# Optimization experiments

Hardware: AMD Instinct MI355X
Metric: run time of the kernel (lower is better)

The kernel has to match this reference:

```python
import jax, jax.numpy as jnp
import numpy as np

N_LAYERS = 3
N_HEADS = 8
N_HIDDEN = 16  # hidden_dim // n_heads
HIDDEN = 128
SLOPE = 0.2


def setup_inputs() -> dict:
    key = jax.random.key(0)
    ks = jax.random.split(key, 7)
    B, N, Din, Dh = 4, 512, 2, HIDDEN
    node_features = jax.random.normal(ks[0], (B, N, Din), dtype=jnp.float32)
    adj = jax.random.randint(ks[1], (B, N, N), 0, 2).astype(jnp.int32)
    adj = jnp.maximum(adj, jnp.eye(N, dtype=jnp.int32)[None])  # self loops -> no empty softmax rows
    s = 1.0 / np.sqrt(Dh)
    W_in = jax.random.normal(ks[2], (Din, Dh), dtype=jnp.float32) * (1.0 / np.sqrt(Din))
    W_l = jax.random.normal(ks[3], (N_LAYERS, Dh, N_HEADS * N_HIDDEN), dtype=jnp.float32) * s
    W_r = jax.random.normal(ks[4], (N_LAYERS, Dh, N_HEADS * N_HIDDEN), dtype=jnp.float32) * s
    attn_a = jax.random.normal(ks[5], (N_LAYERS, N_HIDDEN), dtype=jnp.float32) * (1.0 / np.sqrt(N_HIDDEN))
    W_out = jax.random.normal(ks[6], (Dh, 1), dtype=jnp.float32) * s
    return {"node_features": node_features, "adj": adj, "W_in": W_in,
            "W_l": W_l, "W_r": W_r, "attn_a": attn_a, "W_out": W_out}


def _gatv2_layer(h, adj, Wl, Wr, a):
    # h: [B,N,Dh]; adj: [B,N,N] int; Wl/Wr: [Dh, H*F]; a: [F]
    B, N, _ = h.shape
    g_l = (h @ Wl).reshape(B, N, N_HEADS, N_HIDDEN)
    g_r = (h @ Wr).reshape(B, N, N_HEADS, N_HIDDEN)
    # torch: g_sum[b,i,j] = g_l[b,j] + g_r[b,i]  (repeat vs repeat_interleave)
    g_sum = g_r[:, :, None, :, :] + g_l[:, None, :, :, :]  # [B,N,N,H,F]
    e = jnp.einsum('bijhf,f->bijh', jax.nn.leaky_relu(g_sum, SLOPE), a)  # [B,N,N,H]
    e = jnp.where(adj[..., None] == 0, -jnp.inf, e)
    att = jax.nn.softmax(e, axis=2)  # softmax over neighbors j
    out = jnp.einsum('bijh,bjhf->bihf', att, g_r)  # aggregate g_r (per source)
    return out.reshape(B, N, N_HEADS * N_HIDDEN)


def reference(node_features, adj, W_in, W_l, W_r, attn_a, W_out):
    h = node_features @ W_in  # [B,N,128]
    for i in range(N_LAYERS):
        h = _gatv2_layer(h, adj, W_l[i], W_r[i], attn_a[i])
    return h @ W_out  # [B,N,1]
```

## Files before the change

### kernel.cpp

```cpp
#include <hip/hip_runtime.h>
#include <hip/hip_bf16.h>
#include <cstdint>
#include <math.h>

#define NB 4
#define NN 512
#define DH 128
#define NHEADS 8
#define NHID 16
#define SLOPE 0.2f
#define ITILE 32
#define SENTINEL -1e30f

__global__ __launch_bounds__(256) void pack_adj_kernel(
    const int* __restrict__ adj, uint32_t* __restrict__ adjb)
{
    const int t   = threadIdx.x;
    const int row = blockIdx.x * 16 + (t >> 4);
    const int w   = t & 15;
    const int4* p = (const int4*)(adj + (size_t)row * NN + w * 32);
    uint32_t m = 0;
#pragma unroll
    for (int c = 0; c < 8; ++c) {
        const int4 v = p[c];
        m |= (v.x != 0 ? 1u : 0u) << (c * 4 + 0);
        m |= (v.y != 0 ? 1u : 0u) << (c * 4 + 1);
        m |= (v.z != 0 ? 1u : 0u) << (c * 4 + 2);
        m |= (v.w != 0 ? 1u : 0u) << (c * 4 + 3);
    }
    adjb[(size_t)row * 16 + w] = m;
}

__global__ __launch_bounds__(256) void proj_kernel(
    const float* __restrict__ h, const float* __restrict__ X,
    const float* __restrict__ Win,
    const float* __restrict__ Wl, const float* __restrict__ Wr,
    float* __restrict__ gl, float* __restrict__ gr)
{
    __shared__ __align__(16) float s_h[8][DH];
    const int bn0 = blockIdx.x * 8;
    const int b   = bn0 >> 9;
    const int n0  = bn0 & 511;
    const int t   = threadIdx.x;

    if (X) {
        if (t < DH) {
            const float w0 = Win[t], w1 = Win[DH + t];
#pragma unroll
            for (int r = 0; r < 8; ++r) {
                const float x0 = X[(bn0 + r) * 2 + 0];
                const float x1 = X[(bn0 + r) * 2 + 1];
                s_h[r][t] = x0 * w0 + x1 * w1;
            }
        }
    } else {
        for (int idx = t; idx < 8 * DH; idx += 256)
            s_h[idx >> 7][idx & 127] = h[(size_t)bn0 * DH + idx];
    }
    __syncthreads();

    const float* W = (t < DH) ? Wl : Wr;
    float*       g = (t < DH) ? gl : gr;
    const int f128 = t & 127;
    float acc[8] = {};
    for (int k = 0; k < DH; k += 4) {
        const float w0 = W[(k + 0) * DH + f128];
        const float w1 = W[(k + 1) * DH + f128];
        const float w2 = W[(k + 2) * DH + f128];
        const float w3 = W[(k + 3) * DH + f128];
#pragma unroll
        for (int r = 0; r < 8; ++r) {
            const float4 hv = *(const float4*)&s_h[r][k];
            acc[r] += hv.x * w0 + hv.y * w1 + hv.z * w2 + hv.w * w3;
        }
    }
    const int hh = f128 >> 4, f = f128 & 15;
    float* dst = g + ((size_t)(b * NHEADS + hh) * NN + n0) * NHID + f;
#pragma unroll
    for (int r = 0; r < 8; ++r)
        dst[r * NHID] = acc[r];
}

__global__ __launch_bounds__(512) void attn_kernel(
    const float* __restrict__ gl, const float* __restrict__ gr,
    const uint32_t* __restrict__ adjb, const float* __restrict__ a_vec,
    float* __restrict__ h_out,
    const float* __restrict__ Wout, float* __restrict__ out)
{
    __shared__ __align__(16) float smem[17504];
    float* s_gl  = smem;
    float* s_gr  = smem + 8192;
    float* s_acc = smem;
    float* s_m   = smem + 16384;
    float* s_l   = smem + 16912;
    float* s_M   = smem + 17440;
    float* s_inv = smem + 17472;

    const int blk = blockIdx.x;
    const int it  = blk & 15;
    const int bh  = blk >> 4;
    const int b   = bh >> 3;
    const int hh  = bh & 7;
    const int i0  = it * ITILE;
    const int t   = threadIdx.x;
    const int il  = t & 31;
    const int js  = t >> 5;

    {
        const float4* pgl = (const float4*)(gl + (size_t)bh * NN * NHID);
        const float4* pgr = (const float4*)(gr + (size_t)bh * NN * NHID);
        float4* dl = (float4*)s_gl;
        float4* dr = (float4*)s_gr;
#pragma unroll
        for (int k = 0; k < 4; ++k) {
            dl[k * 512 + t] = pgl[k * 512 + t];
            dr[k * 512 + t] = pgr[k * 512 + t];
        }
    }
    float a[16];
    {
        const float4* pa = (const float4*)a_vec;
#pragma unroll
        for (int q = 0; q < 4; ++q) {
            const float4 v = pa[q];
            a[4*q] = v.x; a[4*q+1] = v.y; a[4*q+2] = v.z; a[4*q+3] = v.w;
        }
    }
    const uint32_t mask = adjb[((size_t)(b * NN + i0 + il)) * 16 + js];
    __syncthreads();

    float gri[16];
    {
        const float4* pr = (const float4*)(s_gr + (i0 + il) * NHID);
#pragma unroll
        for (int q = 0; q < 4; ++q) {
            const float4 v = pr[q];
            gri[4*q] = v.x; gri[4*q+1] = v.y; gri[4*q+2] = v.z; gri[4*q+3] = v.w;
        }
    }

    float m = SENTINEL, l = 0.f;
    float acc[16];
#pragma unroll
    for (int f = 0; f < 16; ++f) acc[f] = 0.f;

    const int jbase = js * 32;
    for (int jc = 0; jc < 32; jc += 4) {
        float sc[4];
#pragma unroll
        for (int k = 0; k < 4; ++k) {
            const int jj = jc + k;
            const float4* pg = (const float4*)(s_gl + (jbase + jj) * NHID);
            float s = 0.f;
#pragma unroll
            for (int q = 0; q < 4; ++q) {
                const float4 g = pg[q];
                float v;
                v = g.x + gri[4*q+0]; v = fmaxf(v, SLOPE * v); s += v * a[4*q+0];
                v = g.y + gri[4*q+1]; v = fmaxf(v, SLOPE * v); s += v * a[4*q+1];
                v = g.z + gri[4*q+2]; v = fmaxf(v, SLOPE * v); s += v * a[4*q+2];
                v = g.w + gri[4*q+3]; v = fmaxf(v, SLOPE * v); s += v * a[4*q+3];
            }
            sc[k] = ((mask >> jj) & 1u) ? s : SENTINEL;
        }
        const float m4   = fmaxf(fmaxf(sc[0], sc[1]), fmaxf(sc[2], sc[3]));
        const float newm = fmaxf(m, m4);
        const float corr = __expf(m - newm);
        l *= corr;
#pragma unroll
        for (int f = 0; f < 16; ++f) acc[f] *= corr;
        float p[4];
#pragma unroll
        for (int k = 0; k < 4; ++k) p[k] = __expf(sc[k] - newm);
        l += p[0] + p[1] + p[2] + p[3];
#pragma unroll
        for (int k = 0; k < 4; ++k) {
            const float4* pg = (const float4*)(s_gr + (jbase + jc + k) * NHID);
#pragma unroll
            for (int q = 0; q < 4; ++q) {
                const float4 g = pg[q];
                acc[4*q+0] += p[k] * g.x; acc[4*q+1] += p[k] * g.y;
                acc[4*q+2] += p[k] * g.z; acc[4*q+3] += p[k] * g.w;
            }
        }
        m = newm;
    }

    s_m[js * 33 + il] = m;
    s_l[js * 33 + il] = l;
    __syncthreads();

    if (t < 32) {
        float M = SENTINEL;
#pragma unroll
        for (int k = 0; k < 16; ++k) M = fmaxf(M, s_m[k * 33 + t]);
        float L = 0.f;
#pragma unroll
        for (int k = 0; k < 16; ++k) L += s_l[k * 33 + t] * __expf(s_m[k * 33 + t] - M);
        s_M[t]   = M;
        s_inv[t] = 1.f / L;
    }
    __syncthreads();

    {
        const float scale = __expf(m - s_M[il]) * s_inv[il];
        float* dst = s_acc + (js * 32 + il) * 17;
#pragma unroll
        for (int f = 0; f < 16; ++f) dst[f] = acc[f] * scale;
    }
    __syncthreads();

    {
        const int i = t >> 4, f = t & 15;
        float o = 0.f;
#pragma unroll
        for (int k = 0; k < 16; ++k) o += s_acc[(k * 32 + i) * 17 + f];
        if (Wout) {
            float v = o * Wout[hh * NHID + f];
#pragma unroll
            for (int off = 8; off; off >>= 1) v += __shfl_xor(v, off);
            if (f == 0) atomicAdd(out + b * NN + i0 + i, v);
        } else {
            h_out[((size_t)(b * NN + i0 + i)) * DH + hh * NHID + f] = o;
        }
    }
}

extern "C" void kernel_launch(void* const* d_in, const int* in_sizes, int n_in,
                              void* d_out, int out_size, void* d_ws, size_t ws_size,
                              hipStream_t stream) {
    const float* X    = (const float*)d_in[0];
    const int*   adj  = (const int*)  d_in[1];
    const float* Win  = (const float*)d_in[2];
    const float* Wl   = (const float*)d_in[3];
    const float* Wr   = (const float*)d_in[4];
    const float* Aa   = (const float*)d_in[5];
    const float* Wout = (const float*)d_in[6];
    float* out = (float*)d_out;

    float*    ws   = (float*)d_ws;
    float*    h    = ws;
    float*    gl   = ws + 262144;
    float*    gr   = ws + 524288;
    uint32_t* adjb = (uint32_t*)(ws + 786432);

    pack_adj_kernel<<<NB * NN / 16, 256, 0, stream>>>(adj, adjb);
    hipMemsetAsync(out, 0, (size_t)out_size * sizeof(float), stream);

    for (int l = 0; l < 3; ++l) {
        proj_kernel<<<NB * NN / 8, 256, 0, stream>>>(
            h, (l == 0) ? X : nullptr, Win,
            Wl + (size_t)l * DH * DH, Wr + (size_t)l * DH * DH, gl, gr);
        const bool last = (l == 2);
        attn_kernel<<<NB * NHEADS * (NN / ITILE), 512, 0, stream>>>(
            gl, gr, adjb, Aa + l * NHID, h,
            last ? Wout : nullptr, out);
    }
}
```

Measured before the change: 180.5 us.

## Rewrite GATv2 attention with abs-based leaky-relu, 64-row tiles, two-pass softmax

Uses the identity leaky_relu(v) = 0.6 v + 0.4 |v| (slope 0.2) to pull the linear term out as precomputed per-node dot products with a, leaving only fabs+fma per element. Each thread now handles two query rows (ITILE 64), so each shared-memory g_l/g_r load is reused twice and there are half as many blocks, each reloading the head's g tensors. The online-softmax rescaling is replaced by a plain two-pass max/exp over 32 register-held scores. The final reduction staging uses an XOR-swizzled layout. Register pressure rises (two score arrays of 32 plus two accumulators), and launch_bounds(512,2) may cause spills.

```diff
diff --git a/kernel.cpp b/kernel.cpp
--- a/kernel.cpp
+++ b/kernel.cpp
@@ -1,5 +1,4 @@
 #include <hip/hip_runtime.h>
-#include <hip/hip_bf16.h>
 #include <cstdint>
 #include <math.h>
 
@@ -9,7 +8,7 @@
 #define NHEADS 8
 #define NHID 16
 #define SLOPE 0.2f
-#define ITILE 32
+#define ITILE 64
 #define SENTINEL -1e30f
 
 __global__ __launch_bounds__(256) void pack_adj_kernel(
@@ -81,147 +80,199 @@
         dst[r * NHID] = acc[r];
 }
 
-__global__ __launch_bounds__(512) void attn_kernel(
+__global__ __launch_bounds__(512, 2) void attn_kernel(
     const float* __restrict__ gl, const float* __restrict__ gr,
     const uint32_t* __restrict__ adjb, const float* __restrict__ a_vec,
     float* __restrict__ h_out,
     const float* __restrict__ Wout, float* __restrict__ out)
 {
-    __shared__ __align__(16) float smem[17504];
+    __shared__ __align__(16) float smem[19616];
     float* s_gl  = smem;
     float* s_gr  = smem + 8192;
     float* s_acc = smem;
-    float* s_m   = smem + 16384;
-    float* s_l   = smem + 16912;
-    float* s_M   = smem + 17440;
-    float* s_inv = smem + 17472;
+    float* s_dgl = smem + 16384;
+    float* s_dgr = smem + 16896;
+    float* s_m   = smem + 17408;
+    float* s_l   = smem + 18448;
+    float* s_M   = smem + 19488;
+    float* s_inv = smem + 19552;
 
     const int blk = blockIdx.x;
-    const int it  = blk & 15;
-    const int bh  = blk >> 4;
+    const int it  = blk & 7;
+    const int bh  = blk >> 3;
     const int b   = bh >> 3;
     const int hh  = bh & 7;
     const int i0  = it * ITILE;
     const int t   = threadIdx.x;
     const int il  = t & 31;
     const int js  = t >> 5;
+    const int r0  = i0 + il;
+    const int r1  = r0 + 32;
+
+    const float4* pgl = (const float4*)(gl + (size_t)bh * NN * NHID);
+    const float4* pgr = (const float4*)(gr + (size_t)bh * NN * NHID);
+    float4 rl[4], rr[4];
+#pragma unroll
+    for (int k = 0; k < 4; ++k) { rl[k] = pgl[k * 512 + t]; rr[k] = pgr[k * 512 + t]; }
+
+    const uint32_t mask0 = adjb[((size_t)(b * NN + r0)) * 16 + js];
+    const uint32_t mask1 = adjb[((size_t)(b * NN + r1)) * 16 + js];
+
+    float gri0[16], gri1[16];
+#pragma unroll
+    for (int q = 0; q < 4; ++q) {
+        const float4 v0 = pgr[r0 * 4 + q];
+        const float4 v1 = pgr[r1 * 4 + q];
+        gri0[4*q+0] = v0.x; gri0[4*q+1] = v0.y; gri0[4*q+2] = v0.z; gri0[4*q+3] = v0.w;
+        gri1[4*q+0] = v1.x; gri1[4*q+1] = v1.y; gri1[4*q+2] = v1.z; gri1[4*q+3] = v1.w;
+    }
+
+    float a[16];
+#pragma unroll
+    for (int q = 0; q < 4; ++q) {
+        const float4 v = ((const float4*)a_vec)[q];
+        a[4*q+0] = v.x; a[4*q+1] = v.y; a[4*q+2] = v.z; a[4*q+3] = v.w;
+    }
 
     {
-        const float4* pgl = (const float4*)(gl + (size_t)bh * NN * NHID);
-        const float4* pgr = (const float4*)(gr + (size_t)bh * NN * NHID);
         float4* dl = (float4*)s_gl;
         float4* dr = (float4*)s_gr;
 #pragma unroll
+        for (int k = 0; k < 4; ++k) { dl[k * 512 + t] = rl[k]; dr[k * 512 + t] = rr[k]; }
+    }
+
+    {
+        const float4 aq = ((const float4*)a_vec)[t & 3];
+#pragma unroll
         for (int k = 0; k < 4; ++k) {
-            dl[k * 512 + t] = pgl[k * 512 + t];
-            dr[k * 512 + t] = pgr[k * 512 + t];
-        }
-    }
-    float a[16];
-    {
-        const float4* pa = (const float4*)a_vec;
+            float pl = rl[k].x * aq.x + rl[k].y * aq.y + rl[k].z * aq.z + rl[k].w * aq.w;
+            float pr = rr[k].x * aq.x + rr[k].y * aq.y + rr[k].z * aq.z + rr[k].w * aq.w;
+            pl += __shfl_xor(pl, 1); pl += __shfl_xor(pl, 2);
+            pr += __shfl_xor(pr, 1); pr += __shfl_xor(pr, 2);
+            if ((t & 3) == 0) {
+                const int row = k * 128 + (t >> 2);
+                s_dgl[row] = pl;
+                s_dgr[row] = pr;
+            }
+        }
+    }
+    __syncthreads();
+
+    const float c0 = 0.6f * s_dgr[r0];
+    const float c1 = 0.6f * s_dgr[r1];
+    const int jbase = js * 32;
+    float sc0[32], sc1[32];
+#pragma unroll
+    for (int jj = 0; jj < 32; ++jj) {
+        const int j = jbase + jj;
+        const float4* pg = (const float4*)(s_gl + j * NHID);
+        const float dj = s_dgl[j];
+        float s0 = 0.f, s1 = 0.f;
 #pragma unroll
         for (int q = 0; q < 4; ++q) {
-            const float4 v = pa[q];
-            a[4*q] = v.x; a[4*q+1] = v.y; a[4*q+2] = v.z; a[4*q+3] = v.w;
-        }
-    }
-    const uint32_t mask = adjb[((size_t)(b * NN + i0 + il)) * 16 + js];
-    __syncthreads();
-
-    float gri[16];
-    {
-        const float4* pr = (const float4*)(s_gr + (i0 + il) * NHID);
+            const float4 g = pg[q];
+            float v;
+            v = g.x + gri0[4*q+0]; s0 = fmaf(a[4*q+0], fabsf(v), s0);
+            v = g.y + gri0[4*q+1]; s0 = fmaf(a[4*q+1], fabsf(v), s0);
+            v = g.z + gri0[4*q+2]; s0 = fmaf(a[4*q+2], fabsf(v), s0);
+            v = g.w + gri0[4*q+3]; s0 = fmaf(a[4*q+3], fabsf(v), s0);
+            v = g.x + gri1[4*q+0]; s1 = fmaf(a[4*q+0], fabsf(v), s1);
+            v = g.y + gri1[4*q+1]; s1 = fmaf(a[4*q+1], fabsf(v), s1);
+            v = g.z + gri1[4*q+2]; s1 = fmaf(a[4*q+2], fabsf(v), s1);
+            v = g.w + gri1[4*q+3]; s1 = fmaf(a[4*q+3], fabsf(v), s1);
+        }
+        const float b0 = fmaf(0.6f, dj, c0);
+        const float b1 = fmaf(0.6f, dj, c1);
+        sc0[jj] = ((mask0 >> jj) & 1u) ? fmaf(0.4f, s0, b0) : SENTINEL;
+        sc1[jj] = ((mask1 >> jj) & 1u) ? fmaf(0.4f, s1, b1) : SENTINEL;
+    }
+
+    float m0 = sc0[0], m1 = sc1[0];
+#pragma unroll
+    for (int jj = 1; jj < 32; ++jj) { m0 = fmaxf(m0, sc0[jj]); m1 = fmaxf(m1, sc1[jj]); }
+    float l0 = 0.f, l1 = 0.f;
+#pragma unroll
+    for (int jj = 0; jj < 32; ++jj) {
+        sc0[jj] = __expf(sc0[jj] - m0); l0 += sc0[jj];
+        sc1[jj] = __expf(sc1[jj] - m1); l1 += sc1[jj];
+    }
+    s_m[js * 65 + il]      = m0;
+    s_m[js * 65 + il + 32] = m1;
+    s_l[js * 65 + il]      = l0;
+    s_l[js * 65 + il + 32] = l1;
+
+    float acc0[16], acc1[16];
+#pragma unroll
+    for (int f = 0; f < 16; ++f) { acc0[f] = 0.f; acc1[f] = 0.f; }
+#pragma unroll
+    for (int jj = 0; jj < 32; ++jj) {
+        const float4* pg = (const float4*)(s_gr + (jbase + jj) * NHID);
+        const float p0 = sc0[jj], p1 = sc1[jj];
 #pragma unroll
         for (int q = 0; q < 4; ++q) {
-            const float4 v = pr[q];
-            gri[4*q] = v.x; gri[4*q+1] = v.y; gri[4*q+2] = v.z; gri[4*q+3] = v.w;
-        }
-    }
-
-    float m = SENTINEL, l = 0.f;
-    float acc[16];
-#pragma unroll
-    for (int f = 0; f < 16; ++f) acc[f] = 0.f;
-
-    const int jbase = js * 32;
-    for (int jc = 0; jc < 32; jc += 4) {
-        float sc[4];
-#pragma unroll
-        for (int k = 0; k < 4; ++k) {
-            const int jj = jc + k;
-            const float4* pg = (const float4*)(s_gl + (jbase + jj) * NHID);
-            float s = 0.f;
-#pragma unroll
-            for (int q = 0; q < 4; ++q) {
-                const float4 g = pg[q];
-                float v;
-                v = g.x + gri[4*q+0]; v = fmaxf(v, SLOPE * v); s += v * a[4*q+0];
-                v = g.y + gri[4*q+1]; v = fmaxf(v, SLOPE * v); s += v * a[4*q+1];
-                v = g.z + gri[4*q+2]; v = fmaxf(v, SLOPE * v); s += v * a[4*q+2];
-                v = g.w + gri[4*q+3]; v = fmaxf(v, SLOPE * v); s += v * a[4*q+3];
-            }
-            sc[k] = ((mask >> jj) & 1u) ? s : SENTINEL;
-        }
-        const float m4   = fmaxf(fmaxf(sc[0], sc[1]), fmaxf(sc[2], sc[3]));
-        const float newm = fmaxf(m, m4);
-        const float corr = __expf(m - newm);
-        l *= corr;
-#pragma unroll
-        for (int f = 0; f < 16; ++f) acc[f] *= corr;
-        float p[4];
-#pragma unroll
-        for (int k = 0; k < 4; ++k) p[k] = __expf(sc[k] - newm);
-        l += p[0] + p[1] + p[2] + p[3];
-#pragma unroll
-        for (int k = 0; k < 4; ++k) {
-            const float4* pg = (const float4*)(s_gr + (jbase + jc + k) * NHID);
-#pragma unroll
-            for (int q = 0; q < 4; ++q) {
-                const float4 g = pg[q];
-                acc[4*q+0] += p[k] * g.x; acc[4*q+1] += p[k] * g.y;
-                acc[4*q+2] += p[k] * g.z; acc[4*q+3] += p[k] * g.w;
-            }
-        }
-        m = newm;
-    }
-
-    s_m[js * 33 + il] = m;
-    s_l[js * 33 + il] = l;
-    __syncthreads();
-
-    if (t < 32) {
+            const float4 g = pg[q];
+            acc0[4*q+0] = fmaf(p0, g.x, acc0[4*q+0]);
+            acc0[4*q+1] = fmaf(p0, g.y, acc0[4*q+1]);
+            acc0[4*q+2] = fmaf(p0, g.z, acc0[4*q+2]);
+            acc0[4*q+3] = fmaf(p0, g.w, acc0[4*q+3]);
+            acc1[4*q+0] = fmaf(p1, g.x, acc1[4*q+0]);
+            acc1[4*q+1] = fmaf(p1, g.y, acc1[4*q+1]);
+            acc1[4*q+2] = fmaf(p1, g.z, acc1[4*q+2]);
+            acc1[4*q+3] = fmaf(p1, g.w, acc1[4*q+3]);
+        }
+    }
+    __syncthreads();
+
+    if (t < 64) {
         float M = SENTINEL;
 #pragma unroll
-        for (int k = 0; k < 16; ++k) M = fmaxf(M, s_m[k * 33 + t]);
+        for (int k = 0; k < 16; ++k) M = fmaxf(M, s_m[k * 65 + t]);
         float L = 0.f;
 #pragma unroll
-        for (int k = 0; k < 16; ++k) L += s_l[k * 33 + t] * __expf(s_m[k * 33 + t] - M);
+        for (int k = 0; k < 16; ++k) L += s_l[k * 65 + t] * __expf(s_m[k * 65 + t] - M);
         s_M[t]   = M;
         s_inv[t] = 1.f / L;
     }
     __syncthreads();
 
     {
-        const float scale = __expf(m - s_M[il]) * s_inv[il];
-        float* dst = s_acc + (js * 32 + il) * 17;
-#pragma unroll
-        for (int f = 0; f < 16; ++f) dst[f] = acc[f] * scale;
+        const float k0 = __expf(m0 - s_M[il])      * s_inv[il];
+        const float k1 = __expf(m1 - s_M[il + 32]) * s_inv[il + 32];
+        const int swz = il & 3;
+        float* base_a = s_acc + js * 1024;
+#pragma unroll
+        for (int q = 0; q < 4; ++q) {
+            float4 v0, v1;
+            v0.x = acc0[4*q+0] * k0; v0.y = acc0[4*q+1] * k0;
+            v0.z = acc0[4*q+2] * k0; v0.w = acc0[4*q+3] * k0;
+            v1.x = acc1[4*q+0] * k1; v1.y = acc1[4*q+1] * k1;
+            v1.z = acc1[4*q+2] * k1; v1.w = acc1[4*q+3] * k1;
+            *(float4*)(base_a + il * 16        + 4 * (q ^ swz)) = v0;
+            *(float4*)(base_a + (il + 32) * 16 + 4 * (q ^ swz)) = v1;
+        }
     }
     __syncthreads();
 
     {
-        const int i = t >> 4, f = t & 15;
-        float o = 0.f;
-#pragma unroll
-        for (int k = 0; k < 16; ++k) o += s_acc[(k * 32 + i) * 17 + f];
-        if (Wout) {
-            float v = o * Wout[hh * NHID + f];
-#pragma unroll
-            for (int off = 8; off; off >>= 1) v += __shfl_xor(v, off);
-            if (f == 0) atomicAdd(out + b * NN + i0 + i, v);
-        } else {
-            h_out[((size_t)(b * NN + i0 + i)) * DH + hh * NHID + f] = o;
+        const int i  = t >> 4;
+        const int f  = t & 15;
+        const int e  = f & 3, qf = f >> 2;
+#pragma unroll
+        for (int r = 0; r < 2; ++r) {
+            const int lr = i + r * 32;
+            const int w  = lr * 16 + 4 * (qf ^ (lr & 3)) + e;
+            float o = 0.f;
+#pragma unroll
+            for (int k = 0; k < 16; ++k) o += s_acc[k * 1024 + w];
+            const int grow = i0 + lr;
+            if (Wout) {
+                float v = o * Wout[hh * NHID + f];
+#pragma unroll
+                for (int off = 8; off; off >>= 1) v += __shfl_xor(v, off);
+                if (f == 0) atomicAdd(out + b * NN + grow, v);
+            } else {
+                h_out[((size_t)(b * NN + grow)) * DH + hh * NHID + f] = o;
+            }
         }
     }
 }
```

Measured after the change: 161.0 us. 10.8% less time.
